# Kernel optimization log

Measured on AMD Instinct MI355X. Metric: run time of the kernel, lower is better.

Reference implementation:

```python
import jax, jax.numpy as jnp
import numpy as np

NUM_HEADS = 16


def setup_inputs() -> dict:
    key = jax.random.key(0)
    ks = jax.random.split(key, 5)
    B, S, D = 2, 2048, 1024
    scale = 0.02
    return {
        "x": jax.random.normal(ks[0], (B, S, D), dtype=jnp.float32),
        "Wq": jax.random.normal(ks[1], (D, D), dtype=jnp.float32) * scale,
        "Wk": jax.random.normal(ks[2], (D, D), dtype=jnp.float32) * scale,
        "Wv": jax.random.normal(ks[3], (D, D), dtype=jnp.float32) * scale,
        "Wo": jax.random.normal(ks[4], (D, D), dtype=jnp.float32) * scale,
        "bo": jnp.zeros((D,), dtype=jnp.float32),
    }


def reference(x, Wq, Wk, Wv, Wo, bo):
    B, S, D = x.shape
    H = NUM_HEADS
    Dh = D // H
    # project and split heads -> [B, H, S, Dh]
    q = (x @ Wq).reshape(B, S, H, Dh).transpose(0, 2, 1, 3)
    k = (x @ Wk).reshape(B, S, H, Dh).transpose(0, 2, 1, 3)
    v = (x @ Wv).reshape(B, S, H, Dh).transpose(0, 2, 1, 3)
    # full causal attention scores [B, H, S, S]
    scores = jnp.einsum("bhqd,bhkd->bhqk", q, k)
    causal_mask = jnp.triu(jnp.ones((S, S), dtype=bool), k=1)
    scores = jnp.where(causal_mask, -jnp.inf, scores)
    attn = jax.nn.softmax(scores / jnp.sqrt(jnp.float32(Dh)), axis=-1)
    ctx = jnp.einsum("bhqk,bhkd->bhqd", attn, v)
    ctx = ctx.transpose(0, 2, 1, 3).reshape(B, S, D)
    return ctx @ Wo + bo
```

## Files before the change

kernel.cpp:

```cpp
#include <hip/hip_runtime.h>
#include <hip/hip_bf16.h>
#include <math.h>

typedef __bf16 bf16_t;
typedef bf16_t bf16x4 __attribute__((ext_vector_type(4)));
typedef bf16_t bf16x8 __attribute__((ext_vector_type(8)));
typedef float f32x4 __attribute__((ext_vector_type(4)));
typedef unsigned int u32;
typedef u32 u32x2 __attribute__((ext_vector_type(2)));
typedef u32 u32x4 __attribute__((ext_vector_type(4)));

#define MFMA16(a, b, c) __builtin_amdgcn_mfma_f32_16x16x32_bf16(a, b, c, 0, 0, 0)
#define NEG_BIG (-1e30f)
#define QSCALE 0.18033688f

#define GLL16(gp, lp)                                                          \
    __builtin_amdgcn_global_load_lds(                                          \
        (const __attribute__((address_space(1))) unsigned int*)(gp),           \
        (__attribute__((address_space(3))) unsigned int*)(lp), 16, 0, 0)


__global__ __launch_bounds__(256) void prep(const float* __restrict__ x,
                                            const float* __restrict__ Wq,
                                            const float* __restrict__ Wk,
                                            const float* __restrict__ Wv,
                                            const float* __restrict__ Wo,
                                            bf16_t* __restrict__ Xb,
                                            bf16_t* __restrict__ WTqkv,
                                            bf16_t* __restrict__ WoT) {
    __shared__ float tile[32][33];
    const int z = blockIdx.z;
    const int tx = threadIdx.x, ty = threadIdx.y;
    if (z == 4) {
        int i0 = (((blockIdx.y * 32 + blockIdx.x) * 256) + ty * 32 + tx) * 4;
        for (int j = 0; j < 4; j++) {
            int i = i0 + j * 1048576;
            float4 v = *(const float4*)(x + i);
            Xb[i + 0] = (bf16_t)v.x;
            Xb[i + 1] = (bf16_t)v.y;
            Xb[i + 2] = (bf16_t)v.z;
            Xb[i + 3] = (bf16_t)v.w;
        }
    } else {
        const float* W = (z == 0) ? Wq : (z == 1) ? Wk : (z == 2) ? Wv : Wo;
        bf16_t* WT = (z < 3) ? (WTqkv + (size_t)z * 1048576) : WoT;
        int bx = blockIdx.x * 32, by = blockIdx.y * 32;
        for (int i = 0; i < 32; i += 8)
            tile[ty + i][tx] = W[(size_t)(by + ty + i) * 1024 + bx + tx];
        __syncthreads();
        for (int i = 0; i < 32; i += 8)
            WT[(size_t)(bx + ty + i) * 1024 + by + tx] = (bf16_t)tile[tx][ty + i];
    }
}

__global__ __launch_bounds__(256) void gemm_qkv(const bf16_t* __restrict__ X,
                                                const bf16_t* __restrict__ WT,
                                                bf16_t* __restrict__ Qd,
                                                bf16_t* __restrict__ Kd,
                                                bf16_t* __restrict__ Vd) {
    __shared__ bf16_t AsmF[2][128 * 64];
    __shared__ bf16_t BsmF[2][128 * 64];
    const int bid = blockIdx.x;
    const int logical = (bid & 7) * 96 + (bid >> 3);
    const int which = logical >> 8;
    const int rem = logical & 255;
    const bf16_t* Wt = WT + (size_t)which * 1024 * 1024;
    const int bm = (rem >> 3) * 128;
    const int bn = (rem & 7) * 128;
    const int tid = threadIdx.x;
    const int wave = tid >> 6, lane = tid & 63;
    const int wm = (wave >> 1) * 64, wn = (wave & 1) * 64;
    const int col = lane & 15, quad = lane >> 4;
    const int cswz = col & 7;
    const int lr8 = lane >> 3;
    const int jg = (lane & 7) ^ lr8;

    const int srow = wave * 32 + lr8;
    const bf16_t* gA = X  + (size_t)(bm + srow) * 1024 + jg * 8;
    const bf16_t* gB = Wt + (size_t)(bn + srow) * 1024 + jg * 8;

    auto stage = [&](int k0, int bsel) {
        bf16_t* lA = AsmF[bsel] + wave * 2048;
        bf16_t* lB = BsmF[bsel] + wave * 2048;
        for (int j = 0; j < 4; j++) {
            GLL16(gA + (size_t)j * 8192 + k0, lA + j * 512);
            GLL16(gB + (size_t)j * 8192 + k0, lB + j * 512);
        }
    };

    stage(0, 0);

    f32x4 acc[4][4] = {};

    for (int t = 0; t < 16; t++) {
        __syncthreads();
        if (t + 1 < 16) stage((t + 1) * 64, (t + 1) & 1);
        const bf16_t* Ab = AsmF[t & 1];
        const bf16_t* Bb = BsmF[t & 1];
        for (int ks = 0; ks < 2; ks++) {
            bf16x8 af[4], bfr[4];
            for (int mi = 0; mi < 4; mi++)
                af[mi] = *(const bf16x8*)&Ab[(wm + mi * 16 + col) * 64 +
                                             (((ks << 2) + quad) ^ cswz) * 8];
            for (int ni = 0; ni < 4; ni++)
                bfr[ni] = *(const bf16x8*)&Bb[(wn + ni * 16 + col) * 64 +
                                              (((ks << 2) + quad) ^ cswz) * 8];
            if (which != 2) {
                for (int mi = 0; mi < 4; mi++)
                    for (int ni = 0; ni < 4; ni++)
                        acc[mi][ni] = MFMA16(af[mi], bfr[ni], acc[mi][ni]);
            } else {
                for (int mi = 0; mi < 4; mi++)
                    for (int ni = 0; ni < 4; ni++)
                        acc[mi][ni] = MFMA16(bfr[ni], af[mi], acc[mi][ni]);
            }
        }
    }

    if (which != 2) {
        const float sc = (which == 0) ? QSCALE : 1.0f;
        for (int mi = 0; mi < 4; mi++) {
            for (int ni = 0; ni < 4; ni++) {
                int mbase = bm + wm + mi * 16 + quad * 4;
                int n = bn + wn + ni * 16 + col;
                int h = n >> 6, dh = n & 63;
                for (int r = 0; r < 4; r++) {
                    int m = mbase + r;
                    int b = m >> 11, s = m & 2047;
                    size_t bh = (size_t)b * 16 + h;
                    bf16_t val = (bf16_t)(acc[mi][ni][r] * sc);
                    if (which == 0) Qd[(bh * 2048 + s) * 64 + dh] = val;
                    else            Kd[(bh * 2048 + s) * 64 + dh] = val;
                }
            }
        }
    } else {
        for (int mi = 0; mi < 4; mi++) {
            for (int ni = 0; ni < 4; ni++) {
                int nbase = bn + wn + ni * 16 + quad * 4;
                int m = bm + wm + mi * 16 + col;
                int b = m >> 11, s = m & 2047;
                for (int r = 0; r < 4; r++) {
                    int n = nbase + r;
                    int h = n >> 6, dh = n & 63;
                    size_t bh = (size_t)b * 16 + h;
                    Vd[(bh * 64 + dh) * 2048 + s] = (bf16_t)acc[mi][ni][r];
                }
            }
        }
    }
}

__global__ __launch_bounds__(128) void attn(const bf16_t* __restrict__ Q,
                                            const bf16_t* __restrict__ K,
                                            const bf16_t* __restrict__ VT,
                                            bf16_t* __restrict__ CTX) {
    __shared__ bf16_t KsF[2 * 64 * 64];
    __shared__ bf16_t VsF[2 * 64 * 64];

    const int bidx = blockIdx.x;
    const int bh = bidx & 31;
    const int qt = 31 - (bidx >> 5);
    const int tid = threadIdx.x;
    const int wave = tid >> 6, lane = tid & 63;
    const int col = lane & 15, quad = lane >> 4;
    const int cswz = col & 7;
    const int lr8 = lane >> 3;
    const int jg = (lane & 7) ^ lr8;

    const bf16_t* Qb = Q + (size_t)bh * 2048 * 64;
    const bf16_t* Kb = K + (size_t)bh * 2048 * 64;
    const bf16_t* Vb = VT + (size_t)bh * 64 * 2048;

    const int strow = wave * 32 + lr8;
    const bf16_t* gK = Kb + (size_t)strow * 64 + jg * 8;
    const bf16_t* gV = Vb + (size_t)strow * 2048 + jg * 8;

    const int b_ = bh >> 4, h_ = bh & 15;

    bf16x8 ones;
    for (int i = 0; i < 8; i++) ones[i] = (bf16_t)1.0f;

    auto stage = [&](int k0, int bsel) {
        bf16_t* lK = KsF + bsel * 4096 + wave * 2048;
        bf16_t* lV = VsF + bsel * 4096 + wave * 2048;
        for (int j = 0; j < 4; j++) {
            GLL16(gK + (size_t)(k0 + j * 8) * 64, lK + j * 512);
            GLL16(gV + (size_t)(k0 + j * 8 * 2048), lV + j * 512);
        }
    };

    stage(0, 0);

    const int q0 = qt * 64;
    const int qrA = q0 + wave * 32 + col;
    const bf16x8 qfA0 = *(const bf16x8*)&Qb[(size_t)qrA * 64 + quad * 8];
    const bf16x8 qfA1 = *(const bf16x8*)&Qb[(size_t)qrA * 64 + 32 + quad * 8];
    const bf16x8 qfB0 = *(const bf16x8*)&Qb[(size_t)(qrA + 16) * 64 + quad * 8];
    const bf16x8 qfB1 = *(const bf16x8*)&Qb[(size_t)(qrA + 16) * 64 + 32 + quad * 8];

    f32x4 o[2][4] = {};
    f32x4 accl[2] = {};

    const int iA = (col | ((quad & 1) << 5)) << 2;
    const bool hi = (quad & 2) != 0;

    const int nt = qt + 1;
    for (int g = 0; g < nt; g++) {
        __syncthreads();
        if (g + 1 < nt) stage((g + 1) * 64, (g + 1) & 1);

        const int bsel = g & 1;
        const bf16_t* Kbuf = KsF + bsel * 4096;
        const bf16_t* Vbuf = VsF + bsel * 4096;
        const bool diag = (g == qt);

        u32x2 pwd[2][4];
#pragma unroll
        for (int ksub = 0; ksub < 4; ksub++) {
            bf16x8 a0 = *(const bf16x8*)&Kbuf[(ksub * 16 + col) * 64 +
                                              (quad ^ cswz) * 8];
            bf16x8 a1 = *(const bf16x8*)&Kbuf[(ksub * 16 + col) * 64 +
                                              ((4 + quad) ^ cswz) * 8];
#pragma unroll
            for (int G = 0; G < 2; G++) {
                f32x4 z = {};
                z = MFMA16(a0, G ? qfB0 : qfA0, z);
                z = MFMA16(a1, G ? qfB1 : qfA1, z);
                if (diag) {
                    int qloc = wave * 32 + G * 16 + col;
                    for (int r = 0; r < 4; r++) {
                        int lk = ksub * 16 + quad * 4 + r;
                        if (lk > qloc) z[r] = NEG_BIG;
                    }
                }
                bf16x4 pw;
#pragma unroll
                for (int r = 0; r < 4; r++)
                    pw[r] = (bf16_t)__builtin_amdgcn_exp2f(z[r]);
                pwd[G][ksub] = __builtin_bit_cast(u32x2, pw);
            }
        }

#pragma unroll
        for (int ck = 0; ck < 2; ck++) {
            bf16x8 vf[4];
#pragma unroll
            for (int d = 0; d < 4; d++)
                vf[d] = *(const bf16x8*)&Vbuf[(d * 16 + col) * 64 +
                                              (((ck << 2) + quad) ^ cswz) * 8];
#pragma unroll
            for (int G = 0; G < 2; G++) {
                u32x2 sA = pwd[G][2 * ck], sB = pwd[G][2 * ck + 1];
                int w0a = __builtin_amdgcn_ds_bpermute(iA,      (int)sA.x);
                int w0b = __builtin_amdgcn_ds_bpermute(iA,      (int)sB.x);
                int w1a = __builtin_amdgcn_ds_bpermute(iA,      (int)sA.y);
                int w1b = __builtin_amdgcn_ds_bpermute(iA,      (int)sB.y);
                int w2a = __builtin_amdgcn_ds_bpermute(iA + 64, (int)sA.x);
                int w2b = __builtin_amdgcn_ds_bpermute(iA + 64, (int)sB.x);
                int w3a = __builtin_amdgcn_ds_bpermute(iA + 64, (int)sA.y);
                int w3b = __builtin_amdgcn_ds_bpermute(iA + 64, (int)sB.y);
                u32x4 pu = {(u32)(hi ? w0b : w0a), (u32)(hi ? w1b : w1a),
                            (u32)(hi ? w2b : w2a), (u32)(hi ? w3b : w3a)};
                bf16x8 pf = __builtin_bit_cast(bf16x8, pu);

                accl[G] = MFMA16(pf, ones, accl[G]);
                for (int d = 0; d < 4; d++)
                    o[G][d] = MFMA16(pf, vf[d], o[G][d]);
            }
        }
    }

#pragma unroll
    for (int G = 0; G < 2; G++) {
        for (int r = 0; r < 4; r++) {
            float rl = __builtin_amdgcn_rcpf(fmaxf(accl[G][r], 1e-20f));
            int s = q0 + wave * 32 + G * 16 + quad * 4 + r;
            for (int d = 0; d < 4; d++) {
                CTX[((size_t)(b_ * 2048 + s)) * 1024 + h_ * 64 + d * 16 + col] =
                    (bf16_t)(o[G][d][r] * rl);
            }
        }
    }
}

__global__ __launch_bounds__(256) void gemm_out(const bf16_t* __restrict__ X,
                                                const bf16_t* __restrict__ WT,
                                                const float* __restrict__ BO,
                                                float* __restrict__ OUT) {
    __shared__ bf16_t AsmF[64 * 64];
    __shared__ bf16_t BsmF[128 * 64];
    const int bid = blockIdx.x;
    const int logical = (bid & 7) * 64 + (bid >> 3);
    const int bm = (logical >> 3) * 64;
    const int bn = (logical & 7) * 128;
    const int tid = threadIdx.x;
    const int wave = tid >> 6, lane = tid & 63;
    const int wm = (wave >> 1) * 32, wn = (wave & 1) * 64;
    const int col = lane & 15, quad = lane >> 4;
    const int cswz = col & 7;
    const int lr8 = lane >> 3;
    const int jg = (lane & 7) ^ lr8;

    const int arow = wave * 16 + lr8;
    const int brow = wave * 32 + lr8;
    const bf16_t* gA = X  + (size_t)(bm + arow) * 1024 + jg * 8;
    const bf16_t* gB = WT + (size_t)(bn + brow) * 1024 + jg * 8;
    bf16_t* lA = AsmF + wave * 1024;
    bf16_t* lB = BsmF + wave * 2048;

    f32x4 acc[2][4] = {};

    for (int k0 = 0; k0 < 1024; k0 += 64) {
        for (int j = 0; j < 2; j++)
            GLL16(gA + (size_t)j * 8192 + k0, lA + j * 512);
        for (int j = 0; j < 4; j++)
            GLL16(gB + (size_t)j * 8192 + k0, lB + j * 512);
        __syncthreads();
        for (int ks = 0; ks < 2; ks++) {
            bf16x8 af[2], bfr[4];
            for (int mi = 0; mi < 2; mi++)
                af[mi] = *(const bf16x8*)&AsmF[(wm + mi * 16 + col) * 64 +
                                               (((ks << 2) + quad) ^ cswz) * 8];
            for (int ni = 0; ni < 4; ni++)
                bfr[ni] = *(const bf16x8*)&BsmF[(wn + ni * 16 + col) * 64 +
                                                (((ks << 2) + quad) ^ cswz) * 8];
            for (int mi = 0; mi < 2; mi++)
                for (int ni = 0; ni < 4; ni++)
                    acc[mi][ni] = MFMA16(af[mi], bfr[ni], acc[mi][ni]);
        }
        __syncthreads();
    }

    for (int mi = 0; mi < 2; mi++) {
        for (int ni = 0; ni < 4; ni++) {
            int mbase = bm + wm + mi * 16 + quad * 4;
            int n = bn + wn + ni * 16 + col;
            float bov = BO[n];
            for (int r = 0; r < 4; r++) {
                int m = mbase + r;
                OUT[(size_t)m * 1024 + n] = acc[mi][ni][r] + bov;
            }
        }
    }
}

extern "C" void kernel_launch(void* const* d_in, const int* in_sizes, int n_in,
                              void* d_out, int out_size, void* d_ws, size_t ws_size,
                              hipStream_t stream) {
    const float* x  = (const float*)d_in[0];
    const float* Wq = (const float*)d_in[1];
    const float* Wk = (const float*)d_in[2];
    const float* Wv = (const float*)d_in[3];
    const float* Wo = (const float*)d_in[4];
    const float* bo = (const float*)d_in[5];
    float* out = (float*)d_out;

    const size_t MEG = 1048576;
    bf16_t* base  = (bf16_t*)d_ws;
    bf16_t* Xb    = base;
    bf16_t* WTqkv = base + 4 * MEG;
    bf16_t* WoT   = base + 7 * MEG;
    bf16_t* Qb    = base + 8 * MEG;
    bf16_t* Kb    = base + 12 * MEG;
    bf16_t* Vb    = base + 16 * MEG;
    bf16_t* Cb    = base + 20 * MEG;

    prep<<<dim3(32, 32, 5), dim3(32, 8), 0, stream>>>(x, Wq, Wk, Wv, Wo,
                                                      Xb, WTqkv, WoT);
    gemm_qkv<<<768, 256, 0, stream>>>(Xb, WTqkv, Qb, Kb, Vb);
    attn<<<1024, 128, 0, stream>>>(Qb, Kb, Vb, Cb);
    gemm_out<<<512, 256, 0, stream>>>(Cb, WoT, bo, out);
}
```

Baseline: 183.5 us.

## Split attention key tile across two wave pairs with LDS reduction

The attention block grows from 2 to 4 waves. Each pair of waves takes half of every 64-key tile for the same 32 query rows, which halves the per-wave MFMA and exp work per tile and gives the scheduler more waves to hide latency. The two halves' partial output and row-sum accumulators are combined through shared memory at the end. The cost is extra barriers, an LDS reduction epilogue, and more threads per block, which may lower the number of blocks resident per CU.

```diff
diff --git a/kernel.cpp b/kernel.cpp
--- a/kernel.cpp
+++ b/kernel.cpp
@@ -151,18 +151,20 @@
     }
 }
 
-__global__ __launch_bounds__(128) void attn(const bf16_t* __restrict__ Q,
+__global__ __launch_bounds__(256) void attn(const bf16_t* __restrict__ Q,
                                             const bf16_t* __restrict__ K,
                                             const bf16_t* __restrict__ VT,
                                             bf16_t* __restrict__ CTX) {
-    __shared__ bf16_t KsF[2 * 64 * 64];
-    __shared__ bf16_t VsF[2 * 64 * 64];
+    __shared__ __align__(16) bf16_t SMEM[16384];
+    bf16_t* KsF = SMEM;
+    bf16_t* VsF = SMEM + 8192;
 
     const int bidx = blockIdx.x;
     const int bh = bidx & 31;
     const int qt = 31 - (bidx >> 5);
     const int tid = threadIdx.x;
     const int wave = tid >> 6, lane = tid & 63;
+    const int qhalf = wave & 1, khalf = wave >> 1;
     const int col = lane & 15, quad = lane >> 4;
     const int cswz = col & 7;
     const int lr8 = lane >> 3;
@@ -172,7 +174,7 @@
     const bf16_t* Kb = K + (size_t)bh * 2048 * 64;
     const bf16_t* Vb = VT + (size_t)bh * 64 * 2048;
 
-    const int strow = wave * 32 + lr8;
+    const int strow = wave * 16 + lr8;
     const bf16_t* gK = Kb + (size_t)strow * 64 + jg * 8;
     const bf16_t* gV = Vb + (size_t)strow * 2048 + jg * 8;
 
@@ -182,9 +184,9 @@
     for (int i = 0; i < 8; i++) ones[i] = (bf16_t)1.0f;
 
     auto stage = [&](int k0, int bsel) {
-        bf16_t* lK = KsF + bsel * 4096 + wave * 2048;
-        bf16_t* lV = VsF + bsel * 4096 + wave * 2048;
-        for (int j = 0; j < 4; j++) {
+        bf16_t* lK = KsF + bsel * 4096 + wave * 1024;
+        bf16_t* lV = VsF + bsel * 4096 + wave * 1024;
+        for (int j = 0; j < 2; j++) {
             GLL16(gK + (size_t)(k0 + j * 8) * 64, lK + j * 512);
             GLL16(gV + (size_t)(k0 + j * 8 * 2048), lV + j * 512);
         }
@@ -193,7 +195,7 @@
     stage(0, 0);
 
     const int q0 = qt * 64;
-    const int qrA = q0 + wave * 32 + col;
+    const int qrA = q0 + qhalf * 32 + col;
     const bf16x8 qfA0 = *(const bf16x8*)&Qb[(size_t)qrA * 64 + quad * 8];
     const bf16x8 qfA1 = *(const bf16x8*)&Qb[(size_t)qrA * 64 + 32 + quad * 8];
     const bf16x8 qfB0 = *(const bf16x8*)&Qb[(size_t)(qrA + 16) * 64 + quad * 8];
@@ -215,9 +217,10 @@
         const bf16_t* Vbuf = VsF + bsel * 4096;
         const bool diag = (g == qt);
 
-        u32x2 pwd[2][4];
-#pragma unroll
-        for (int ksub = 0; ksub < 4; ksub++) {
+        u32x2 pwd[2][2];
+#pragma unroll
+        for (int ksl = 0; ksl < 2; ksl++) {
+            const int ksub = khalf * 2 + ksl;
             bf16x8 a0 = *(const bf16x8*)&Kbuf[(ksub * 16 + col) * 64 +
                                               (quad ^ cswz) * 8];
             bf16x8 a1 = *(const bf16x8*)&Kbuf[(ksub * 16 + col) * 64 +
@@ -228,7 +231,7 @@
                 z = MFMA16(a0, G ? qfB0 : qfA0, z);
                 z = MFMA16(a1, G ? qfB1 : qfA1, z);
                 if (diag) {
-                    int qloc = wave * 32 + G * 16 + col;
+                    int qloc = qhalf * 32 + G * 16 + col;
                     for (int r = 0; r < 4; r++) {
                         int lk = ksub * 16 + quad * 4 + r;
                         if (lk > qloc) z[r] = NEG_BIG;
@@ -238,47 +241,66 @@
 #pragma unroll
                 for (int r = 0; r < 4; r++)
                     pw[r] = (bf16_t)__builtin_amdgcn_exp2f(z[r]);
-                pwd[G][ksub] = __builtin_bit_cast(u32x2, pw);
-            }
-        }
-
-#pragma unroll
-        for (int ck = 0; ck < 2; ck++) {
-            bf16x8 vf[4];
-#pragma unroll
+                pwd[G][ksl] = __builtin_bit_cast(u32x2, pw);
+            }
+        }
+
+        bf16x8 vf[4];
+#pragma unroll
+        for (int d = 0; d < 4; d++)
+            vf[d] = *(const bf16x8*)&Vbuf[(d * 16 + col) * 64 +
+                                          (((khalf << 2) + quad) ^ cswz) * 8];
+#pragma unroll
+        for (int G = 0; G < 2; G++) {
+            u32x2 sA = pwd[G][0], sB = pwd[G][1];
+            int w0a = __builtin_amdgcn_ds_bpermute(iA,      (int)sA.x);
+            int w0b = __builtin_amdgcn_ds_bpermute(iA,      (int)sB.x);
+            int w1a = __builtin_amdgcn_ds_bpermute(iA,      (int)sA.y);
+            int w1b = __builtin_amdgcn_ds_bpermute(iA,      (int)sB.y);
+            int w2a = __builtin_amdgcn_ds_bpermute(iA + 64, (int)sA.x);
+            int w2b = __builtin_amdgcn_ds_bpermute(iA + 64, (int)sB.x);
+            int w3a = __builtin_amdgcn_ds_bpermute(iA + 64, (int)sA.y);
+            int w3b = __builtin_amdgcn_ds_bpermute(iA + 64, (int)sB.y);
+            u32x4 pu = {(u32)(hi ? w0b : w0a), (u32)(hi ? w1b : w1a),
+                        (u32)(hi ? w2b : w2a), (u32)(hi ? w3b : w3a)};
+            bf16x8 pf = __builtin_bit_cast(bf16x8, pu);
+
+            accl[G] = MFMA16(pf, ones, accl[G]);
             for (int d = 0; d < 4; d++)
-                vf[d] = *(const bf16x8*)&Vbuf[(d * 16 + col) * 64 +
-                                              (((ck << 2) + quad) ^ cswz) * 8];
-#pragma unroll
-            for (int G = 0; G < 2; G++) {
-                u32x2 sA = pwd[G][2 * ck], sB = pwd[G][2 * ck + 1];
-                int w0a = __builtin_amdgcn_ds_bpermute(iA,      (int)sA.x);
-                int w0b = __builtin_amdgcn_ds_bpermute(iA,      (int)sB.x);
-                int w1a = __builtin_amdgcn_ds_bpermute(iA,      (int)sA.y);
-                int w1b = __builtin_amdgcn_ds_bpermute(iA,      (int)sB.y);
-                int w2a = __builtin_amdgcn_ds_bpermute(iA + 64, (int)sA.x);
-                int w2b = __builtin_amdgcn_ds_bpermute(iA + 64, (int)sB.x);
-                int w3a = __builtin_amdgcn_ds_bpermute(iA + 64, (int)sA.y);
-                int w3b = __builtin_amdgcn_ds_bpermute(iA + 64, (int)sB.y);
-                u32x4 pu = {(u32)(hi ? w0b : w0a), (u32)(hi ? w1b : w1a),
-                            (u32)(hi ? w2b : w2a), (u32)(hi ? w3b : w3a)};
-                bf16x8 pf = __builtin_bit_cast(bf16x8, pu);
-
-                accl[G] = MFMA16(pf, ones, accl[G]);
-                for (int d = 0; d < 4; d++)
-                    o[G][d] = MFMA16(pf, vf[d], o[G][d]);
-            }
-        }
-    }
-
-#pragma unroll
-    for (int G = 0; G < 2; G++) {
-        for (int r = 0; r < 4; r++) {
-            float rl = __builtin_amdgcn_rcpf(fmaxf(accl[G][r], 1e-20f));
-            int s = q0 + wave * 32 + G * 16 + quad * 4 + r;
-            for (int d = 0; d < 4; d++) {
-                CTX[((size_t)(b_ * 2048 + s)) * 1024 + h_ * 64 + d * 16 + col] =
-                    (bf16_t)(o[G][d][r] * rl);
+                o[G][d] = MFMA16(pf, vf[d], o[G][d]);
+        }
+    }
+
+    __syncthreads();
+    float* ex = (float*)SMEM;
+    if (khalf == 1) {
+        float* p = ex + qhalf * 3072 + lane * 48;
+#pragma unroll
+        for (int G = 0; G < 2; G++)
+            for (int d = 0; d < 4; d++)
+                *(f32x4*)(p + (G * 4 + d) * 4) = o[G][d];
+        *(f32x4*)(p + 32) = accl[0];
+        *(f32x4*)(p + 36) = accl[1];
+    }
+    __syncthreads();
+    if (khalf == 0) {
+        float* p = ex + qhalf * 3072 + lane * 48;
+#pragma unroll
+        for (int G = 0; G < 2; G++)
+            for (int d = 0; d < 4; d++)
+                o[G][d] += *(const f32x4*)(p + (G * 4 + d) * 4);
+        accl[0] += *(const f32x4*)(p + 32);
+        accl[1] += *(const f32x4*)(p + 36);
+
+#pragma unroll
+        for (int G = 0; G < 2; G++) {
+            for (int r = 0; r < 4; r++) {
+                float rl = __builtin_amdgcn_rcpf(fmaxf(accl[G][r], 1e-20f));
+                int s = q0 + qhalf * 32 + G * 16 + quad * 4 + r;
+                for (int d = 0; d < 4; d++) {
+                    CTX[((size_t)(b_ * 2048 + s)) * 1024 + h_ * 64 + d * 16 + col] =
+                        (bf16_t)(o[G][d][r] * rl);
+                }
             }
         }
     }
@@ -369,6 +391,6 @@
     prep<<<dim3(32, 32, 5), dim3(32, 8), 0, stream>>>(x, Wq, Wk, Wv, Wo,
                                                       Xb, WTqkv, WoT);
     gemm_qkv<<<768, 256, 0, stream>>>(Xb, WTqkv, Qb, Kb, Vb);
-    attn<<<1024, 128, 0, stream>>>(Qb, Kb, Vb, Cb);
+    attn<<<1024, 256, 0, stream>>>(Qb, Kb, Vb, Cb);
     gemm_out<<<512, 256, 0, stream>>>(Cb, WoT, bo, out);
 }
```

After: 172.8 us. 5.9% less time.
